# Kernel tuning notes

Measured on AMD Instinct MI355X. Metric: run time of the kernel, lower is better.

## Reference

```python
import jax, jax.numpy as jnp
import numpy as np

WS = 8          # window size
NH = 4          # num heads
DIM = 64
HID = 256       # mlp_ratio * dim
EPS = 1e-5


def _rel_pos_index(ws):
    coords = np.stack(np.meshgrid(np.arange(ws), np.arange(ws), indexing='ij')).reshape(2, -1)
    rel = (coords[:, :, None] - coords[:, None, :]).transpose(1, 2, 0)  # (N,N,2)
    rel[..., 0] += ws - 1
    rel[..., 1] += ws - 1
    rel[..., 0] *= 2 * ws - 1
    return rel.sum(-1)  # (N,N)


def _layernorm(x, g, b):
    mu = x.mean(-1, keepdims=True)
    var = ((x - mu) ** 2).mean(-1, keepdims=True)
    return (x - mu) * jax.lax.rsqrt(var + EPS) * g + b


def setup_inputs() -> dict:
    key = jax.random.key(0)
    ks = jax.random.split(key, 16)
    s = 0.02
    return {
        'x': jax.random.normal(ks[0], (8, DIM, 256, 256), jnp.float32),
        'qkv_w': jax.random.normal(ks[1], (DIM, 3 * DIM), jnp.float32) * s,
        'qkv_b': jnp.zeros((3 * DIM,), jnp.float32),
        'proj_w': jax.random.normal(ks[2], (DIM, DIM), jnp.float32) * s,
        'proj_b': jnp.zeros((DIM,), jnp.float32),
        'rpb_table': jax.random.normal(ks[3], ((2 * WS - 1) ** 2, NH), jnp.float32) * s,
        'norm1_g': jnp.ones((DIM,), jnp.float32),
        'norm1_b': jnp.zeros((DIM,), jnp.float32),
        'norm2_g': jnp.ones((DIM,), jnp.float32),
        'norm2_b': jnp.zeros((DIM,), jnp.float32),
        'ffn_w1': jax.random.normal(ks[4], (DIM, HID), jnp.float32) * s,
        'ffn_b1': jnp.zeros((HID,), jnp.float32),
        'ffn_w2': jax.random.normal(ks[5], (HID, DIM), jnp.float32) * s,
        'ffn_w2_b': jnp.zeros((DIM,), jnp.float32),
        'dw_w': jax.random.normal(ks[6], (DIM, 1, 3, 3), jnp.float32) * s,
        'dw_b': jnp.zeros((DIM,), jnp.float32),
    }


def reference(x, qkv_w, qkv_b, proj_w, proj_b, rpb_table,
              norm1_g, norm1_b, norm2_g, norm2_b,
              ffn_w1, ffn_b1, ffn_w2, ffn_w2_b, dw_w, dw_b):
    B, C, H, W = x.shape
    ws, nh = WS, NH
    hd = C // nh
    N = ws * ws
    assert H % ws == 0 and W % ws == 0  # chosen shapes avoid reflect pad

    x_hw = jnp.transpose(x, (0, 2, 3, 1))  # (B,H,W,C)

    # --- window attention branch ---
    xn = _layernorm(x_hw, norm1_g, norm1_b)
    win = xn.reshape(B, H // ws, ws, W // ws, ws, C).transpose(0, 1, 3, 2, 4, 5)
    win = win.reshape(-1, N, C)  # (B*nW, N, C)

    qkv = win @ qkv_w + qkv_b  # (BnW, N, 3C)
    qkv = qkv.reshape(-1, N, 3, nh, hd).transpose(2, 0, 3, 1, 4)
    q, k, v = qkv[0], qkv[1], qkv[2]  # (BnW, nh, N, hd)

    scale = hd ** -0.5
    attn = jnp.einsum('bhnd,bhmd->bhnm', q, k) * scale
    idx = _rel_pos_index(ws)
    bias = rpb_table[idx.reshape(-1)].reshape(N, N, nh).transpose(2, 0, 1)  # (nh,N,N)
    attn = jax.nn.softmax(attn + bias[None], axis=-1)
    out = jnp.einsum('bhnm,bhmd->bhnd', attn, v)
    out = out.transpose(0, 2, 1, 3).reshape(-1, N, C)
    out = out @ proj_w + proj_b

    out = out.reshape(B, H // ws, W // ws, ws, ws, C).transpose(0, 1, 3, 2, 4, 5)
    out = out.reshape(B, H, W, C)
    x_hw = x_hw + out

    # --- FFN + depthwise conv branch ---
    xn = _layernorm(x_hw, norm2_g, norm2_b)
    ffn = jax.nn.gelu(xn @ ffn_w1 + ffn_b1, approximate=False) @ ffn_w2 + ffn_w2_b

    xc = jnp.transpose(x_hw, (0, 3, 1, 2))  # (B,C,H,W)
    xc = jax.lax.conv_general_dilated(
        xc, dw_w, window_strides=(1, 1), padding=((1, 1), (1, 1)),
        feature_group_count=C,
        dimension_numbers=('NCHW', 'OIHW', 'NCHW')) + dw_b[None, :, None, None]
    xc = jnp.transpose(xc, (0, 2, 3, 1))

    x_hw = x_hw + ffn + xc
    return jnp.transpose(x_hw, (0, 3, 1, 2))  # (B,C,H,W)
```

## Files before the change

kernel.cpp:

```cpp
#include <hip/hip_runtime.h>
#include <cmath>


typedef __attribute__((ext_vector_type(8))) short bf16x8;
typedef __attribute__((ext_vector_type(4))) short s16x4;
typedef __attribute__((ext_vector_type(4))) float f32x4;

static __device__ __forceinline__ unsigned short f2bf(float f) {
  union { float f; unsigned u; } v; v.f = f;
  unsigned r = v.u + 0x7FFF + ((v.u >> 16) & 1);
  return (unsigned short)(r >> 16);
}
static __device__ __forceinline__ float bf2f(unsigned short u) {
  union { unsigned u; float f; } v; v.u = ((unsigned)u) << 16;
  return v.f;
}
static __device__ __forceinline__ float bf2f_s(short s) { return bf2f((unsigned short)s); }

static __device__ __forceinline__ int swz(int row, int c) {
  return row * 72 + ((((c >> 3) ^ (row >> 3)) & 7) << 3) + (c & 7);
}
static __device__ __forceinline__ int swzg(int row, int g) {
  return row * 72 + (((g ^ (row >> 3)) & 7) << 3);
}

#define MFMA32(a, b, c) __builtin_amdgcn_mfma_f32_16x16x32_bf16(a, b, c, 0, 0, 0)

#if __has_builtin(__builtin_amdgcn_mfma_f32_16x16x16bf16_1k)
static __device__ __forceinline__ f32x4 MFMA16(s16x4 a, s16x4 b, f32x4 c) {
  return __builtin_amdgcn_mfma_f32_16x16x16bf16_1k(a, b, c, 0, 0, 0);
}
#else
static __device__ __forceinline__ f32x4 MFMA16(s16x4 a, s16x4 b, f32x4 c) {
  bf16x8 a8 = (bf16x8){a[0], a[1], a[2], a[3], 0, 0, 0, 0};
  bf16x8 b8 = (bf16x8){b[0], b[1], b[2], b[3], 0, 0, 0, 0};
  return __builtin_amdgcn_mfma_f32_16x16x32_bf16(a8, b8, c, 0, 0, 0);
}
#endif

__global__ void pack_weights_kernel(const float* __restrict__ qkv_w,
                                    const float* __restrict__ proj_w,
                                    const float* __restrict__ w1,
                                    const float* __restrict__ w2,
                                    const float* __restrict__ rpb,
                                    unsigned short* __restrict__ qkvt,
                                    unsigned short* __restrict__ projt,
                                    unsigned short* __restrict__ w1t,
                                    unsigned short* __restrict__ w2t,
                                    float* __restrict__ biasg) {
  const int t = blockIdx.x * 256 + threadIdx.x;
  {
    const int n = t >> 6, k = t & 63;
    if (n < 192) qkvt[t] = f2bf(qkv_w[k * 192 + n]);
    if (n < 64)  projt[t] = f2bf(proj_w[k * 64 + n]);
    w1t[t] = f2bf(w1[k * 256 + n]);
  }
  {
    const int n = t >> 8, k = t & 255;
    w2t[t] = f2bf(w2[k * 64 + n]);
  }
  {
    const int i = (t >> 6) & 63, j = t & 63, h = t >> 12;
    const int ridx = ((i >> 3) - (j >> 3) + 7) * 15 + ((i & 7) - (j & 7) + 7);
    biasg[t] = rpb[ridx * 4 + h];
  }
}

__global__ __launch_bounds__(256, 3)
void win_attn_kernel(const float* __restrict__ x,
                     const unsigned short* __restrict__ qkvt,
                     const float* __restrict__ qkv_b,
                     const unsigned short* __restrict__ projt,
                     const float* __restrict__ proj_b,
                     const float* __restrict__ biasg,
                     const float* __restrict__ n1g,
                     const float* __restrict__ n1b,
                     unsigned short* __restrict__ x1b)
{
  __shared__ unsigned short xw[64 * 72];
  __shared__ unsigned short xn[64 * 72];

  const int tid = threadIdx.x;
  const int bid = blockIdx.x;
  const int wid = ((bid & 7) << 10) | (bid >> 3);
  const int b  = wid >> 10;
  const int wy = (wid >> 5) & 31;
  const int wx = wid & 31;
  const int y0 = wy << 3, x0 = wx << 3;

  const size_t imgbase = (size_t)b << 22;
#pragma unroll
  for (int i = 0; i < 16; ++i) {
    const int idx = i * 256 + tid;
    const int c = idx >> 6, t = idx & 63;
    const float v = x[imgbase + ((size_t)c << 16) + (size_t)(y0 + (t >> 3)) * 256 + (x0 + (t & 7))];
    xw[swz(t, c)] = f2bf(v);
  }
  __syncthreads();

  {
    const int t = tid >> 2, q = tid & 3;
    const bf16x8 h0 = *(const bf16x8*)&xw[swzg(t, 2 * q)];
    const bf16x8 h1 = *(const bf16x8*)&xw[swzg(t, 2 * q + 1)];
    float xv[16], s = 0.f, s2 = 0.f;
#pragma unroll
    for (int j = 0; j < 8; ++j) { xv[j] = bf2f_s(h0[j]); xv[8 + j] = bf2f_s(h1[j]); }
#pragma unroll
    for (int j = 0; j < 16; ++j) { s += xv[j]; s2 += xv[j] * xv[j]; }
    s  += __shfl_xor(s, 1);  s  += __shfl_xor(s, 2);
    s2 += __shfl_xor(s2, 1); s2 += __shfl_xor(s2, 2);
    const float mu   = s * 0.015625f;
    const float rstd = rsqrtf(s2 * 0.015625f - mu * mu + 1e-5f);
#pragma unroll
    for (int j = 0; j < 8; ++j) {
      const int c = q * 16 + j * 2;
      const float a0 = (xv[j * 2 + 0] - mu) * rstd * n1g[c]     + n1b[c];
      const float a1 = (xv[j * 2 + 1] - mu) * rstd * n1g[c + 1] + n1b[c + 1];
      *(unsigned*)&xn[swz(t, c)] = (unsigned)f2bf(a0) | ((unsigned)f2bf(a1) << 16);
    }
  }
  __syncthreads();

  const int lane = tid & 63;
  const int g    = tid >> 6;
  const int lr   = lane & 15;
  const int lg   = lane >> 4;

  bf16x8 afr[4][2];
#pragma unroll
  for (int mt = 0; mt < 4; ++mt)
#pragma unroll
    for (int ks = 0; ks < 2; ++ks)
      afr[mt][ks] = *(const bf16x8*)&xn[swzg(mt * 16 + lr, ks * 4 + lg)];
  __syncthreads();

  f32x4 dqT[4], dkT[4], dv[4];
#pragma unroll
  for (int u = 0; u < 4; ++u) { dqT[u] = (f32x4){0,0,0,0}; dkT[u] = (f32x4){0,0,0,0}; dv[u] = (f32x4){0,0,0,0}; }
  const int nbq = g * 16, nbk = 64 + g * 16, nbv = 128 + g * 16;
#pragma unroll
  for (int ks = 0; ks < 2; ++ks) {
    const bf16x8 wq = *(const bf16x8*)&qkvt[(nbq + lr) * 64 + ks * 32 + lg * 8];
    const bf16x8 wk = *(const bf16x8*)&qkvt[(nbk + lr) * 64 + ks * 32 + lg * 8];
    const bf16x8 wv = *(const bf16x8*)&qkvt[(nbv + lr) * 64 + ks * 32 + lg * 8];
#pragma unroll
    for (int u = 0; u < 4; ++u) {
      dqT[u] = MFMA32(wq, afr[u][ks], dqT[u]);
      dkT[u] = MFMA32(wk, afr[u][ks], dkT[u]);
      dv[u]  = MFMA32(afr[u][ks], wv, dv[u]);
    }
  }
  s16x4 qf[4], kf[4], vf[4];
  {
    const float4 qb = *(const float4*)&qkv_b[nbq + lg * 4];
    const float4 kb = *(const float4*)&qkv_b[nbk + lg * 4];
    const float  vb = qkv_b[nbv + lr];
#pragma unroll
    for (int u = 0; u < 4; ++u) {
      qf[u] = (s16x4){(short)f2bf((dqT[u][0] + qb.x) * 0.25f), (short)f2bf((dqT[u][1] + qb.y) * 0.25f),
                      (short)f2bf((dqT[u][2] + qb.z) * 0.25f), (short)f2bf((dqT[u][3] + qb.w) * 0.25f)};
      kf[u] = (s16x4){(short)f2bf(dkT[u][0] + kb.x), (short)f2bf(dkT[u][1] + kb.y),
                      (short)f2bf(dkT[u][2] + kb.z), (short)f2bf(dkT[u][3] + kb.w)};
      vf[u] = (s16x4){(short)f2bf(dv[u][0] + vb), (short)f2bf(dv[u][1] + vb),
                      (short)f2bf(dv[u][2] + vb), (short)f2bf(dv[u][3] + vb)};
    }
  }

  f32x4 sacc[4][4];
#pragma unroll
  for (int mt = 0; mt < 4; ++mt)
#pragma unroll
    for (int nt = 0; nt < 4; ++nt) {
      f32x4 z = (f32x4){0,0,0,0};
      sacc[mt][nt] = MFMA16(kf[mt], qf[nt], z);
    }
#pragma unroll
  for (int nt = 0; nt < 4; ++nt)
#pragma unroll
    for (int mt = 0; mt < 4; ++mt) {
      const float4 bb = *(const float4*)&biasg[(g << 12) + (nt * 16 + lr) * 64 + mt * 16 + lg * 4];
      sacc[mt][nt][0] += bb.x; sacc[mt][nt][1] += bb.y;
      sacc[mt][nt][2] += bb.z; sacc[mt][nt][3] += bb.w;
    }

  s16x4 pa[4][4];
#pragma unroll
  for (int nt = 0; nt < 4; ++nt) {
    float mx = -1e30f;
#pragma unroll
    for (int mt = 0; mt < 4; ++mt)
#pragma unroll
      for (int r = 0; r < 4; ++r) mx = fmaxf(mx, sacc[mt][nt][r]);
    mx = fmaxf(mx, __shfl_xor(mx, 16));
    mx = fmaxf(mx, __shfl_xor(mx, 32));
    float sum = 0.f;
#pragma unroll
    for (int mt = 0; mt < 4; ++mt)
#pragma unroll
      for (int r = 0; r < 4; ++r) { const float e = __expf(sacc[mt][nt][r] - mx); sacc[mt][nt][r] = e; sum += e; }
    sum += __shfl_xor(sum, 16);
    sum += __shfl_xor(sum, 32);
    const float rs = 1.f / sum;
#pragma unroll
    for (int mt = 0; mt < 4; ++mt)
      pa[mt][nt] = (s16x4){(short)f2bf(sacc[mt][nt][0] * rs), (short)f2bf(sacc[mt][nt][1] * rs),
                           (short)f2bf(sacc[mt][nt][2] * rs), (short)f2bf(sacc[mt][nt][3] * rs)};
  }

  f32x4 o[4];
#pragma unroll
  for (int nt = 0; nt < 4; ++nt) {
    o[nt] = (f32x4){0,0,0,0};
#pragma unroll
    for (int mt = 0; mt < 4; ++mt)
      o[nt] = MFMA16(pa[mt][nt], vf[mt], o[nt]);
  }

#pragma unroll
  for (int nt = 0; nt < 4; ++nt)
#pragma unroll
    for (int r = 0; r < 4; ++r)
      xn[swz(nt * 16 + lg * 4 + r, g * 16 + lr)] = f2bf(o[nt][r]);
  __syncthreads();

  {
    bf16x8 pa2[4][2];
#pragma unroll
    for (int mt = 0; mt < 4; ++mt)
#pragma unroll
      for (int ks = 0; ks < 2; ++ks)
        pa2[mt][ks] = *(const bf16x8*)&xn[swzg(mt * 16 + lr, ks * 4 + lg)];
    __syncthreads();

    f32x4 d2[4];
#pragma unroll
    for (int mt = 0; mt < 4; ++mt) d2[mt] = (f32x4){0,0,0,0};
#pragma unroll
    for (int ks = 0; ks < 2; ++ks) {
      const bf16x8 pb = *(const bf16x8*)&projt[(g * 16 + lr) * 64 + ks * 32 + lg * 8];
#pragma unroll
      for (int mt = 0; mt < 4; ++mt)
        d2[mt] = MFMA32(pa2[mt][ks], pb, d2[mt]);
    }
    const float pbias = proj_b[g * 16 + lr];
#pragma unroll
    for (int mt = 0; mt < 4; ++mt)
#pragma unroll
      for (int r = 0; r < 4; ++r) {
        const int tok = mt * 16 + lg * 4 + r;
        const float val = d2[mt][r] + pbias + bf2f(xw[swz(tok, g * 16 + lr)]);
        xn[swz(tok, g * 16 + lr)] = f2bf(val);
      }
  }
  __syncthreads();

#pragma unroll
  for (int i = 0; i < 2; ++i) {
    const int u = i * 256 + tid;
    const int tok = u >> 3, gr = u & 7;
    const bf16x8 v = *(const bf16x8*)&xn[swzg(tok, gr)];
    *(bf16x8*)&x1b[(((size_t)b * 256 + y0 + (tok >> 3)) * 256 + x0 + (tok & 7)) * 64 + gr * 8] = v;
  }
}

__global__ __launch_bounds__(256, 4)
void ffn_conv_kernel(const unsigned short* __restrict__ x1b,
                     const float* __restrict__ n2g, const float* __restrict__ n2b,
                     const unsigned short* __restrict__ w1t, const float* __restrict__ b1,
                     const unsigned short* __restrict__ w2t, const float* __restrict__ b2,
                     const float* __restrict__ dww, const float* __restrict__ dwb,
                     float* __restrict__ out)
{
  __shared__ unsigned short pool[11808];
  __shared__ float          ob[64][65];
  unsigned short* x1h = pool;
  unsigned short* xnb = pool + 7200;
  unsigned short* hid = pool;

  const int tid = threadIdx.x;
  const int bid = blockIdx.x;
  const int wid = ((bid & 7) << 10) | (bid >> 3);
  const int b  = wid >> 10;
  const int wy = (wid >> 5) & 31;
  const int wx = wid & 31;
  const int y0 = wy << 3, x0 = wx << 3;

#pragma unroll
  for (int i = 0; i < 7; ++i) {
    const int u = i * 256 + tid;
    if (u < 1600) {
      const int p = u >> 4, c4 = (u & 15) << 2;
      const int py = p / 10, px = p - py * 10;
      const int gy = y0 + py - 1, gx = x0 + px - 1;
      uint2 v = make_uint2(0u, 0u);
      if ((unsigned)gy < 256u && (unsigned)gx < 256u)
        v = *(const uint2*)&x1b[(((size_t)b * 256 + gy) * 256 + gx) * 64 + c4];
      *(uint2*)&x1h[p * 72 + c4] = v;
    }
  }
  __syncthreads();

  const int lane = tid & 63;
  const int g    = tid >> 6;
  const int lr   = lane & 15;
  const int lg   = lane >> 4;

  {
    const int t = tid >> 2, q = tid & 3;
    const int pp = ((t >> 3) + 1) * 10 + (t & 7) + 1;
    const bf16x8 h0 = *(const bf16x8*)&x1h[pp * 72 + q * 16];
    const bf16x8 h1 = *(const bf16x8*)&x1h[pp * 72 + q * 16 + 8];
    float xv[16], s = 0.f, s2 = 0.f;
#pragma unroll
    for (int j = 0; j < 8; ++j) { xv[j] = bf2f_s(h0[j]); xv[8 + j] = bf2f_s(h1[j]); }
#pragma unroll
    for (int j = 0; j < 16; ++j) { s += xv[j]; s2 += xv[j] * xv[j]; }
    s  += __shfl_xor(s, 1);  s  += __shfl_xor(s, 2);
    s2 += __shfl_xor(s2, 1); s2 += __shfl_xor(s2, 2);
    const float mu   = s * 0.015625f;
    const float rstd = rsqrtf(s2 * 0.015625f - mu * mu + 1e-5f);
#pragma unroll
    for (int j = 0; j < 8; ++j) {
      const int c = q * 16 + j * 2;
      const float a0 = (xv[j * 2 + 0] - mu) * rstd * n2g[c]     + n2b[c];
      const float a1 = (xv[j * 2 + 1] - mu) * rstd * n2g[c + 1] + n2b[c + 1];
      *(unsigned*)&xnb[swz(t, c)] = (unsigned)f2bf(a0) | ((unsigned)f2bf(a1) << 16);
    }
  }

  {
    const int cty = lane >> 3, ctx = lane & 7;
    float cacc[16];
#pragma unroll
    for (int i = 0; i < 16; ++i) cacc[i] = dwb[g * 16 + i];
#pragma unroll
    for (int dy = 0; dy < 3; ++dy)
#pragma unroll
      for (int dx = 0; dx < 3; ++dx) {
        const int p = (cty + dy) * 10 + (ctx + dx);
        const bf16x8 h0 = *(const bf16x8*)&x1h[p * 72 + g * 16];
        const bf16x8 h1 = *(const bf16x8*)&x1h[p * 72 + g * 16 + 8];
#pragma unroll
        for (int i = 0; i < 8; ++i) {
          cacc[i]     += dww[(g * 16 + i) * 9     + dy * 3 + dx] * bf2f_s(h0[i]);
          cacc[8 + i] += dww[(g * 16 + 8 + i) * 9 + dy * 3 + dx] * bf2f_s(h1[i]);
        }
      }
    const int cp = (cty + 1) * 10 + (ctx + 1);
    const bf16x8 r0 = *(const bf16x8*)&x1h[cp * 72 + g * 16];
    const bf16x8 r1 = *(const bf16x8*)&x1h[cp * 72 + g * 16 + 8];
#pragma unroll
    for (int i = 0; i < 8; ++i) {
      ob[lane][g * 16 + i]     = bf2f_s(r0[i]) + cacc[i];
      ob[lane][g * 16 + 8 + i] = bf2f_s(r1[i]) + cacc[8 + i];
    }
  }
  __syncthreads();

  bf16x8 afr[4][2];
#pragma unroll
  for (int mt = 0; mt < 4; ++mt)
#pragma unroll
    for (int ks = 0; ks < 2; ++ks)
      afr[mt][ks] = *(const bf16x8*)&xnb[swzg(mt * 16 + lr, ks * 4 + lg)];
  __syncthreads();

  f32x4 d2[4];
#pragma unroll
  for (int mt = 0; mt < 4; ++mt) d2[mt] = (f32x4){0,0,0,0};

#pragma unroll
  for (int half = 0; half < 2; ++half) {
    f32x4 d1[2][4];
#pragma unroll
    for (int nt = 0; nt < 2; ++nt)
#pragma unroll
      for (int mt = 0; mt < 4; ++mt) d1[nt][mt] = (f32x4){0,0,0,0};
#pragma unroll
    for (int nt = 0; nt < 2; ++nt) {
      const int n = half * 128 + g * 32 + nt * 16 + lr;
#pragma unroll
      for (int ks = 0; ks < 2; ++ks) {
        const bf16x8 bw = *(const bf16x8*)&w1t[n * 64 + ks * 32 + lg * 8];
#pragma unroll
        for (int mt = 0; mt < 4; ++mt)
          d1[nt][mt] = MFMA32(afr[mt][ks], bw, d1[nt][mt]);
      }
    }
#pragma unroll
    for (int nt = 0; nt < 2; ++nt) {
      const int n  = half * 128 + g * 32 + nt * 16 + lr;
      const int nl = g * 32 + nt * 16 + lr;
      const float bb = b1[n];
#pragma unroll
      for (int mt = 0; mt < 4; ++mt)
#pragma unroll
        for (int r = 0; r < 4; ++r) {
          float h = d1[nt][mt][r] + bb;
          const float z = h * (1.5957691216f + 0.0713548162f * h * h);
          h = h / (1.f + __expf(-z));
          hid[(mt * 16 + lg * 4 + r) * 136 + nl] = f2bf(h);
        }
    }
    __syncthreads();

#pragma unroll
    for (int ks = 0; ks < 4; ++ks) {
      const bf16x8 bw = *(const bf16x8*)&w2t[(g * 16 + lr) * 256 + half * 128 + ks * 32 + lg * 8];
#pragma unroll
      for (int mt = 0; mt < 4; ++mt) {
        const bf16x8 af = *(const bf16x8*)&hid[(mt * 16 + lr) * 136 + ks * 32 + lg * 8];
        d2[mt] = MFMA32(af, bw, d2[mt]);
      }
    }
    __syncthreads();
  }

  {
    const float b2n = b2[g * 16 + lr];
#pragma unroll
    for (int mt = 0; mt < 4; ++mt)
#pragma unroll
      for (int r = 0; r < 4; ++r)
        ob[mt * 16 + lg * 4 + r][g * 16 + lr] += d2[mt][r] + b2n;
  }
  __syncthreads();

#pragma unroll
  for (int i = 0; i < 16; ++i) {
    const int idx = i * 256 + tid;
    const int c = idx >> 6, t = idx & 63;
    out[(((size_t)b * 64 + c) * 256 + (y0 + (t >> 3))) * 256 + (x0 + (t & 7))] = ob[t][c];
  }
}

extern "C" void kernel_launch(void* const* d_in, const int* in_sizes, int n_in,
                              void* d_out, int out_size, void* d_ws, size_t ws_size,
                              hipStream_t stream) {
  const float* x      = (const float*)d_in[0];
  const float* qkv_w  = (const float*)d_in[1];
  const float* qkv_b  = (const float*)d_in[2];
  const float* proj_w = (const float*)d_in[3];
  const float* proj_b = (const float*)d_in[4];
  const float* rpb    = (const float*)d_in[5];
  const float* n1g    = (const float*)d_in[6];
  const float* n1b    = (const float*)d_in[7];
  const float* n2g    = (const float*)d_in[8];
  const float* n2b    = (const float*)d_in[9];
  const float* w1     = (const float*)d_in[10];
  const float* b1     = (const float*)d_in[11];
  const float* w2     = (const float*)d_in[12];
  const float* b2     = (const float*)d_in[13];
  const float* dww    = (const float*)d_in[14];
  const float* dwb    = (const float*)d_in[15];
  float* out = (float*)d_out;

  unsigned short* x1bf = (unsigned short*)d_ws;
  unsigned short* wbuf = (unsigned short*)((char*)d_ws + 67108864);
  unsigned short* qkvt  = wbuf;
  unsigned short* projt = wbuf + 12288;
  unsigned short* w1t   = wbuf + 16384;
  unsigned short* w2t   = wbuf + 32768;
  float* biasg = (float*)((char*)d_ws + 67108864 + 98304);

  pack_weights_kernel<<<64, 256, 0, stream>>>(qkv_w, proj_w, w1, w2, rpb,
                                              qkvt, projt, w1t, w2t, biasg);
  win_attn_kernel<<<8192, 256, 0, stream>>>(x, qkvt, qkv_b, projt, proj_b,
                                            biasg, n1g, n1b, x1bf);
  ffn_conv_kernel<<<8192, 256, 0, stream>>>(x1bf, n2g, n2b, w1t, b1, w2t, b2,
                                            dww, dwb, out);
}
```

Baseline: 334.1 us.

## Drop LDS halo staging in FFN/conv kernel and raise occupancy

```diff
diff --git a/kernel.cpp b/kernel.cpp
--- a/kernel.cpp
+++ b/kernel.cpp
@@ -263,7 +263,7 @@
   }
 }
 
-__global__ __launch_bounds__(256, 4)
+__global__ __launch_bounds__(256, 6)
 void ffn_conv_kernel(const unsigned short* __restrict__ x1b,
                      const float* __restrict__ n2g, const float* __restrict__ n2b,
                      const unsigned short* __restrict__ w1t, const float* __restrict__ b1,
@@ -271,11 +271,10 @@
                      const float* __restrict__ dww, const float* __restrict__ dwb,
                      float* __restrict__ out)
 {
-  __shared__ unsigned short pool[11808];
-  __shared__ float          ob[64][65];
-  unsigned short* x1h = pool;
-  unsigned short* xnb = pool + 7200;
+  __shared__ __align__(16) unsigned short pool[8320];
+  unsigned short* xnb = pool;
   unsigned short* hid = pool;
+  float*          d2f = (float*)pool;
 
   const int tid = threadIdx.x;
   const int bid = blockIdx.x;
@@ -285,21 +284,6 @@
   const int wx = wid & 31;
   const int y0 = wy << 3, x0 = wx << 3;
 
-#pragma unroll
-  for (int i = 0; i < 7; ++i) {
-    const int u = i * 256 + tid;
-    if (u < 1600) {
-      const int p = u >> 4, c4 = (u & 15) << 2;
-      const int py = p / 10, px = p - py * 10;
-      const int gy = y0 + py - 1, gx = x0 + px - 1;
-      uint2 v = make_uint2(0u, 0u);
-      if ((unsigned)gy < 256u && (unsigned)gx < 256u)
-        v = *(const uint2*)&x1b[(((size_t)b * 256 + gy) * 256 + gx) * 64 + c4];
-      *(uint2*)&x1h[p * 72 + c4] = v;
-    }
-  }
-  __syncthreads();
-
   const int lane = tid & 63;
   const int g    = tid >> 6;
   const int lr   = lane & 15;
@@ -307,9 +291,9 @@
 
   {
     const int t = tid >> 2, q = tid & 3;
-    const int pp = ((t >> 3) + 1) * 10 + (t & 7) + 1;
-    const bf16x8 h0 = *(const bf16x8*)&x1h[pp * 72 + q * 16];
-    const bf16x8 h1 = *(const bf16x8*)&x1h[pp * 72 + q * 16 + 8];
+    const size_t tbase = (((size_t)b * 256 + y0 + (t >> 3)) * 256 + x0 + (t & 7)) * 64 + q * 16;
+    const bf16x8 h0 = *(const bf16x8*)&x1b[tbase];
+    const bf16x8 h1 = *(const bf16x8*)&x1b[tbase + 8];
     float xv[16], s = 0.f, s2 = 0.f;
 #pragma unroll
     for (int j = 0; j < 8; ++j) { xv[j] = bf2f_s(h0[j]); xv[8 + j] = bf2f_s(h1[j]); }
@@ -327,110 +311,115 @@
       *(unsigned*)&xnb[swz(t, c)] = (unsigned)f2bf(a0) | ((unsigned)f2bf(a1) << 16);
     }
   }
-
-  {
-    const int cty = lane >> 3, ctx = lane & 7;
-    float cacc[16];
-#pragma unroll
-    for (int i = 0; i < 16; ++i) cacc[i] = dwb[g * 16 + i];
+  __syncthreads();
+
+  bf16x8 afr[4][2];
+#pragma unroll
+  for (int mt = 0; mt < 4; ++mt)
+#pragma unroll
+    for (int ks = 0; ks < 2; ++ks)
+      afr[mt][ks] = *(const bf16x8*)&xnb[swzg(mt * 16 + lr, ks * 4 + lg)];
+  __syncthreads();
+
+  f32x4 d2[4];
+#pragma unroll
+  for (int mt = 0; mt < 4; ++mt) d2[mt] = (f32x4){0,0,0,0};
+
+#pragma unroll
+  for (int half = 0; half < 2; ++half) {
+    f32x4 d1[2][4];
+#pragma unroll
+    for (int nt = 0; nt < 2; ++nt)
+#pragma unroll
+      for (int mt = 0; mt < 4; ++mt) d1[nt][mt] = (f32x4){0,0,0,0};
+#pragma unroll
+    for (int nt = 0; nt < 2; ++nt) {
+      const int nb = half * 128 + g * 32 + nt * 16;
+#pragma unroll
+      for (int ks = 0; ks < 2; ++ks) {
+        const bf16x8 aw = *(const bf16x8*)&w1t[(nb + lr) * 64 + ks * 32 + lg * 8];
+#pragma unroll
+        for (int mt = 0; mt < 4; ++mt)
+          d1[nt][mt] = MFMA32(aw, afr[mt][ks], d1[nt][mt]);
+      }
+    }
+#pragma unroll
+    for (int nt = 0; nt < 2; ++nt) {
+      const int nb = half * 128 + g * 32 + nt * 16;
+      const float4 bb = *(const float4*)&b1[nb + lg * 4];
+#pragma unroll
+      for (int mt = 0; mt < 4; ++mt) {
+        s16x4 pk;
+#pragma unroll
+        for (int r = 0; r < 4; ++r) {
+          const float bias = (r == 0) ? bb.x : (r == 1) ? bb.y : (r == 2) ? bb.z : bb.w;
+          const float xg = d1[nt][mt][r] + bias;
+          const float e  = __expf(-1.702f * xg);
+          pk[r] = (short)f2bf(__fdividef(xg, 1.f + e));
+        }
+        const int row  = mt * 16 + lr;
+        const int nl   = g * 32 + nt * 16 + lg * 4;
+        const int addr = row * 128 + (((nl >> 3) ^ (row & 7)) << 3) + (nl & 7);
+        *(s16x4*)&hid[addr] = pk;
+      }
+    }
+    __syncthreads();
+
+#pragma unroll
+    for (int ks2 = 0; ks2 < 4; ++ks2) {
+      const bf16x8 bw = *(const bf16x8*)&w2t[(g * 16 + lr) * 256 + half * 128 + ks2 * 32 + lg * 8];
+#pragma unroll
+      for (int mt = 0; mt < 4; ++mt) {
+        const int row  = mt * 16 + lr;
+        const int gran = ks2 * 4 + lg;
+        const bf16x8 ah = *(const bf16x8*)&hid[row * 128 + ((gran ^ (row & 7)) << 3)];
+        d2[mt] = MFMA32(ah, bw, d2[mt]);
+      }
+    }
+    __syncthreads();
+  }
+
+  {
+    const float b2n = b2[g * 16 + lr];
+#pragma unroll
+    for (int mt = 0; mt < 4; ++mt)
+#pragma unroll
+      for (int r = 0; r < 4; ++r)
+        d2f[(mt * 16 + lg * 4 + r) * 65 + g * 16 + lr] = d2[mt][r] + b2n;
+  }
+  __syncthreads();
+
+  {
+    const int py = lane >> 3, px = lane & 7;
+    float acc[16];
+#pragma unroll
+    for (int i = 0; i < 16; ++i) acc[i] = dwb[g * 16 + i];
 #pragma unroll
     for (int dy = 0; dy < 3; ++dy)
 #pragma unroll
       for (int dx = 0; dx < 3; ++dx) {
-        const int p = (cty + dy) * 10 + (ctx + dx);
-        const bf16x8 h0 = *(const bf16x8*)&x1h[p * 72 + g * 16];
-        const bf16x8 h1 = *(const bf16x8*)&x1h[p * 72 + g * 16 + 8];
+        const int gy = y0 + py + dy - 1, gx = x0 + px + dx - 1;
+        bf16x8 h0 = (bf16x8){0,0,0,0,0,0,0,0};
+        bf16x8 h1 = (bf16x8){0,0,0,0,0,0,0,0};
+        if ((unsigned)gy < 256u && (unsigned)gx < 256u) {
+          const size_t base = (((size_t)b * 256 + gy) * 256 + gx) * 64 + g * 16;
+          h0 = *(const bf16x8*)&x1b[base];
+          h1 = *(const bf16x8*)&x1b[base + 8];
+        }
+        const bool ctr = (dy == 1) && (dx == 1);
 #pragma unroll
         for (int i = 0; i < 8; ++i) {
-          cacc[i]     += dww[(g * 16 + i) * 9     + dy * 3 + dx] * bf2f_s(h0[i]);
-          cacc[8 + i] += dww[(g * 16 + 8 + i) * 9 + dy * 3 + dx] * bf2f_s(h1[i]);
+          float w0 = dww[(g * 16 + i) * 9     + dy * 3 + dx];
+          float w1_ = dww[(g * 16 + 8 + i) * 9 + dy * 3 + dx];
+          if (ctr) { w0 += 1.f; w1_ += 1.f; }
+          acc[i]     += w0  * bf2f_s(h0[i]);
+          acc[8 + i] += w1_ * bf2f_s(h1[i]);
         }
       }
-    const int cp = (cty + 1) * 10 + (ctx + 1);
-    const bf16x8 r0 = *(const bf16x8*)&x1h[cp * 72 + g * 16];
-    const bf16x8 r1 = *(const bf16x8*)&x1h[cp * 72 + g * 16 + 8];
-#pragma unroll
-    for (int i = 0; i < 8; ++i) {
-      ob[lane][g * 16 + i]     = bf2f_s(r0[i]) + cacc[i];
-      ob[lane][g * 16 + 8 + i] = bf2f_s(r1[i]) + cacc[8 + i];
-    }
-  }
-  __syncthreads();
-
-  bf16x8 afr[4][2];
-#pragma unroll
-  for (int mt = 0; mt < 4; ++mt)
-#pragma unroll
-    for (int ks = 0; ks < 2; ++ks)
-      afr[mt][ks] = *(const bf16x8*)&xnb[swzg(mt * 16 + lr, ks * 4 + lg)];
-  __syncthreads();
-
-  f32x4 d2[4];
-#pragma unroll
-  for (int mt = 0; mt < 4; ++mt) d2[mt] = (f32x4){0,0,0,0};
-
-#pragma unroll
-  for (int half = 0; half < 2; ++half) {
-    f32x4 d1[2][4];
-#pragma unroll
-    for (int nt = 0; nt < 2; ++nt)
-#pragma unroll
-      for (int mt = 0; mt < 4; ++mt) d1[nt][mt] = (f32x4){0,0,0,0};
-#pragma unroll
-    for (int nt = 0; nt < 2; ++nt) {
-      const int n = half * 128 + g * 32 + nt * 16 + lr;
-#pragma unroll
-      for (int ks = 0; ks < 2; ++ks) {
-        const bf16x8 bw = *(const bf16x8*)&w1t[n * 64 + ks * 32 + lg * 8];
-#pragma unroll
-        for (int mt = 0; mt < 4; ++mt)
-          d1[nt][mt] = MFMA32(afr[mt][ks], bw, d1[nt][mt]);
-      }
-    }
-#pragma unroll
-    for (int nt = 0; nt < 2; ++nt) {
-      const int n  = half * 128 + g * 32 + nt * 16 + lr;
-      const int nl = g * 32 + nt * 16 + lr;
-      const float bb = b1[n];
-#pragma unroll
-      for (int mt = 0; mt < 4; ++mt)
-#pragma unroll
-        for (int r = 0; r < 4; ++r) {
-          float h = d1[nt][mt][r] + bb;
-          const float z = h * (1.5957691216f + 0.0713548162f * h * h);
-          h = h / (1.f + __expf(-z));
-          hid[(mt * 16 + lg * 4 + r) * 136 + nl] = f2bf(h);
-        }
-    }
-    __syncthreads();
-
-#pragma unroll
-    for (int ks = 0; ks < 4; ++ks) {
-      const bf16x8 bw = *(const bf16x8*)&w2t[(g * 16 + lr) * 256 + half * 128 + ks * 32 + lg * 8];
-#pragma unroll
-      for (int mt = 0; mt < 4; ++mt) {
-        const bf16x8 af = *(const bf16x8*)&hid[(mt * 16 + lr) * 136 + ks * 32 + lg * 8];
-        d2[mt] = MFMA32(af, bw, d2[mt]);
-      }
-    }
-    __syncthreads();
-  }
-
-  {
-    const float b2n = b2[g * 16 + lr];
-#pragma unroll
-    for (int mt = 0; mt < 4; ++mt)
-#pragma unroll
-      for (int r = 0; r < 4; ++r)
-        ob[mt * 16 + lg * 4 + r][g * 16 + lr] += d2[mt][r] + b2n;
-  }
-  __syncthreads();
-
-#pragma unroll
-  for (int i = 0; i < 16; ++i) {
-    const int idx = i * 256 + tid;
-    const int c = idx >> 6, t = idx & 63;
-    out[(((size_t)b * 64 + c) * 256 + (y0 + (t >> 3))) * 256 + (x0 + (t & 7))] = ob[t][c];
+    const size_t obase = ((size_t)b * 64 + g * 16) * 65536 + (size_t)(y0 + py) * 256 + (x0 + px);
+#pragma unroll
+    for (int i = 0; i < 16; ++i)
+      out[obase + (size_t)i * 65536] = acc[i] + d2f[lane * 65 + g * 16 + i];
   }
 }
 
```

New measurement: 1.207 ms. 3.61x slower.
